# Performance work log

Measured on AMD Instinct MI355X. Metric: run time of the kernel, lower is better.

Reference implementation:

```python
import jax, jax.numpy as jnp
import numpy as np

B, S, DIM, H = 4, 2048, 1024, 16
DEPTH = DIM // H


def setup_inputs() -> dict:
    key = jax.random.key(0)
    ks = jax.random.split(key, 12)
    s = 0.02
    return {
        "Q": jax.random.normal(ks[0], (B, S, DIM), jnp.float32),
        "K": jax.random.normal(ks[1], (B, S, DIM), jnp.float32),
        "V": jax.random.normal(ks[2], (B, S, DIM), jnp.float32),
        "mask": jax.random.randint(ks[3], (B, 1, 1, S), 0, 2).astype(jnp.float32),
        "Wq": jax.random.normal(ks[4], (DIM, DIM), jnp.float32) * s,
        "bq": jnp.zeros((DIM,), jnp.float32),
        "Wk": jax.random.normal(ks[5], (DIM, DIM), jnp.float32) * s,
        "bk": jnp.zeros((DIM,), jnp.float32),
        "Wv": jax.random.normal(ks[6], (DIM, DIM), jnp.float32) * s,
        "bv": jnp.zeros((DIM,), jnp.float32),
        "Wo": jax.random.normal(ks[7], (DIM, DIM), jnp.float32) * s,
        "bo": jnp.zeros((DIM,), jnp.float32),
    }


def _split_heads(x):
    # [B,S,DIM] -> [B,H,S,DEPTH]
    return x.reshape(x.shape[0], x.shape[1], H, DEPTH).transpose(0, 2, 1, 3)


def reference(Q, K, V, mask, Wq, bq, Wk, bk, Wv, bv, Wo, bo):
    q = _split_heads(Q @ Wq + bq)
    k = _split_heads(K @ Wk + bk)
    v = _split_heads(V @ Wv + bv)
    # scaled dot-product attention; note original scales by sqrt(depth) = last dim of K after split
    logits = jnp.einsum("bhqd,bhkd->bhqk", q, k) / jnp.sqrt(jnp.float32(DEPTH))
    logits = logits + mask * -1e9
    attn = jax.nn.softmax(logits, axis=-1)
    ctx = jnp.einsum("bhqk,bhkd->bhqd", attn, v)
    ctx = ctx.transpose(0, 2, 1, 3).reshape(Q.shape[0], Q.shape[1], DIM)
    return ctx @ Wo + bo
```

## Files before the change

kernel.cpp:

```cpp
#include <hip/hip_runtime.h>

typedef short s16x8 __attribute__((ext_vector_type(8)));
typedef short s16x4 __attribute__((ext_vector_type(4)));
typedef float f32x4 __attribute__((ext_vector_type(4)));

#define MFMA32(a, b, c) __builtin_amdgcn_mfma_f32_16x16x32_bf16((a), (b), (c), 0, 0, 0)

__device__ __forceinline__ void stage16(const unsigned short* g, unsigned short* l) {
#if defined(__HIP_DEVICE_COMPILE__)
  __builtin_amdgcn_global_load_lds((const __attribute__((address_space(1))) unsigned int*)g,
                                   (__attribute__((address_space(3))) unsigned int*)l, 16, 0, 0);
#endif
}

__device__ __forceinline__ unsigned short f2b(float f) {
  unsigned int u = __builtin_bit_cast(unsigned int, f);
  unsigned int r = u + 0x7FFFu + ((u >> 16) & 1u);
  return (unsigned short)(r >> 16);
}
__device__ __forceinline__ unsigned int pk2(float a, float b) {
  return (unsigned int)f2b(a) | ((unsigned int)f2b(b) << 16);
}
__device__ __forceinline__ float fast_exp2(float x) {
#if defined(__HIP_DEVICE_COMPILE__) && __has_builtin(__builtin_amdgcn_exp2f)
  return __builtin_amdgcn_exp2f(x);
#else
  return exp2f(x);
#endif
}

__global__ __launch_bounds__(256) void castq(const float* __restrict__ X,
                                             unsigned short* __restrict__ Y) {
  int i = blockIdx.x * 256 + threadIdx.x;
  float4 f0 = ((const float4*)X)[i * 2];
  float4 f1 = ((const float4*)X)[i * 2 + 1];
  uint4 u;
  u.x = pk2(f0.x, f0.y);
  u.y = pk2(f0.z, f0.w);
  u.z = pk2(f1.x, f1.y);
  u.w = pk2(f1.z, f1.w);
  ((uint4*)Y)[i] = u;
}

__global__ void wtrans(const float* __restrict__ W0, const float* __restrict__ W1,
                       const float* __restrict__ W2, const float* __restrict__ W3,
                       unsigned short* __restrict__ T0, unsigned short* __restrict__ T1,
                       unsigned short* __restrict__ T2, unsigned short* __restrict__ T3) {
  const float* W;
  unsigned short* T;
  switch (blockIdx.z) {
    case 0: W = W0; T = T0; break;
    case 1: W = W1; T = T1; break;
    case 2: W = W2; T = T2; break;
    default: W = W3; T = T3; break;
  }
  __shared__ float tile[32][33];
  const int n0 = blockIdx.x << 5;
  const int k0 = blockIdx.y << 5;
  const int tx = threadIdx.x;
  const int ty = threadIdx.y;
#pragma unroll
  for (int j = 0; j < 4; ++j)
    tile[ty + 8 * j][tx] = W[(size_t)(k0 + ty + 8 * j) * 1024 + n0 + tx];
  __syncthreads();
#pragma unroll
  for (int j = 0; j < 4; ++j)
    T[(size_t)(n0 + ty + 8 * j) * 1024 + k0 + tx] = f2b(tile[tx][ty + 8 * j]);
}

template <int MODE>
__global__ __launch_bounds__(256, 2) void gemm_bt(const unsigned short* __restrict__ A,
                                                  const unsigned short* __restrict__ Bt,
                                                  const float* __restrict__ bias,
                                                  void* __restrict__ Cout, float oscale) {
  __shared__ __align__(16) unsigned short As[128 * 32];
  __shared__ __align__(16) unsigned short Bs[128 * 32];
  const int n0 = blockIdx.x * 128;
  const int m0 = blockIdx.y * 128;
  const int tid = threadIdx.x;
  const int w = tid >> 6;
  const int lane = tid & 63;
  const int lr = lane & 15;
  const int lg = lane >> 4;
  const int wm = (w >> 1) << 6;
  const int wn = (w & 1) << 6;

  const int srow = w * 16 + (lane >> 2);
  const int sseg = lane & 3;
  const unsigned short* Ag0 = A + (size_t)(m0 + srow) * 1024 + sseg * 8;
  const unsigned short* Ag1 = A + (size_t)(m0 + 64 + srow) * 1024 + sseg * 8;
  const unsigned short* Bg0 = Bt + (size_t)(n0 + srow) * 1024 + sseg * 8;
  const unsigned short* Bg1 = Bt + (size_t)(n0 + 64 + srow) * 1024 + sseg * 8;
  unsigned short* Al0 = &As[(w * 16) * 32];
  unsigned short* Al1 = &As[(64 + w * 16) * 32];
  unsigned short* Bl0 = &Bs[(w * 16) * 32];
  unsigned short* Bl1 = &Bs[(64 + w * 16) * 32];

  f32x4 acc[4][4];
#pragma unroll
  for (int i = 0; i < 4; ++i)
#pragma unroll
    for (int j = 0; j < 4; ++j) {
      f32x4 z = {0.f, 0.f, 0.f, 0.f};
      acc[i][j] = z;
    }

  for (int k0 = 0; k0 < 1024; k0 += 32) {
    stage16(Ag0 + k0, Al0);
    stage16(Ag1 + k0, Al1);
    stage16(Bg0 + k0, Bl0);
    stage16(Bg1 + k0, Bl1);
    __syncthreads();
    s16x8 af[4], bfr[4];
#pragma unroll
    for (int mt = 0; mt < 4; ++mt) af[mt] = *(const s16x8*)&As[(wm + mt * 16 + lr) * 32 + lg * 8];
#pragma unroll
    for (int nt = 0; nt < 4; ++nt) bfr[nt] = *(const s16x8*)&Bs[(wn + nt * 16 + lr) * 32 + lg * 8];
#pragma unroll
    for (int mt = 0; mt < 4; ++mt)
#pragma unroll
      for (int nt = 0; nt < 4; ++nt)
        acc[mt][nt] = MFMA32(af[mt], bfr[nt], acc[mt][nt]);
    __syncthreads();
  }

  float bcol[4];
#pragma unroll
  for (int nt = 0; nt < 4; ++nt) bcol[nt] = bias[n0 + wn + nt * 16 + lr];

#pragma unroll
  for (int mt = 0; mt < 4; ++mt)
#pragma unroll
    for (int nt = 0; nt < 4; ++nt)
#pragma unroll
      for (int r = 0; r < 4; ++r) {
        float v = (acc[mt][nt][r] + bcol[nt]) * oscale;
        int row = m0 + wm + mt * 16 + lg * 4 + r;
        int col = n0 + wn + nt * 16 + lr;
        if constexpr (MODE == 0) {
          int b = row >> 11, s = row & 2047, hh = col >> 6, d = col & 63;
          ((unsigned short*)Cout)[(((size_t)(b * 16 + hh) * 2048 + s) << 6) + d] = f2b(v);
        } else if constexpr (MODE == 1) {
          int b = row >> 11, s = row & 2047, hh = col >> 6, d = col & 63;
          ((unsigned short*)Cout)[(((size_t)(b * 16 + hh) * 64 + d) << 11) + s] = f2b(v);
        } else {
          ((float*)Cout)[(size_t)row * 1024 + col] = v;
        }
      }
}

__global__ __launch_bounds__(256, 4) void flash_attn(const unsigned short* __restrict__ qh,
                                                     const unsigned short* __restrict__ kh,
                                                     const unsigned short* __restrict__ vt,
                                                     const float* __restrict__ mask,
                                                     unsigned short* __restrict__ ctx) {
  const float c2 = 1.4426950408889634e9f;
  const int id = blockIdx.x;
  const int bh = id & 63;
  const int qtile = id >> 6;
  const int b = bh >> 4;
  const int h = bh & 15;
  const int q0 = qtile << 7;
  const int tid = threadIdx.x;
  const int w = tid >> 6;
  const int lane = tid & 63;
  const int lr = lane & 15;
  const int lg = lane >> 4;

  __shared__ __align__(16) unsigned short Ks[64 * 64];
  __shared__ __align__(16) unsigned short Vs[64 * 64];

  const unsigned short* qbase = qh + ((size_t)bh * 2048 + q0 + w * 32) * 64;
  const unsigned short* kbase = kh + (size_t)bh * 2048 * 64;
  const unsigned short* vbase = vt + (size_t)bh * 64 * 2048;
  const float* mbase = mask + b * 2048;

  const int rowc = lane >> 3;
  const int gseg = (lane & 7) ^ rowc;
  const unsigned short* kg0 = kbase + (size_t)(w * 16 + rowc) * 64 + gseg * 8;
  const unsigned short* kg1 = kbase + (size_t)(w * 16 + 8 + rowc) * 64 + gseg * 8;
  const unsigned short* vg0 = vbase + (size_t)(w * 16 + rowc) * 2048 + gseg * 8;
  const unsigned short* vg1 = vbase + (size_t)(w * 16 + 8 + rowc) * 2048 + gseg * 8;
  unsigned short* kl0 = &Ks[(w * 16 + 0) * 64];
  unsigned short* kl1 = &Ks[(w * 16 + 8) * 64];
  unsigned short* vl0 = &Vs[(w * 16 + 0) * 64];
  unsigned short* vl1 = &Vs[(w * 16 + 8) * 64];

  s16x8 qf[2][2];
#pragma unroll
  for (int qt = 0; qt < 2; ++qt)
#pragma unroll
    for (int kk = 0; kk < 2; ++kk)
      qf[qt][kk] = *(const s16x8*)(qbase + (qt * 16 + lr) * 64 + kk * 32 + lg * 8);

  const s16x8 ones8 = {(short)0x3F80, (short)0x3F80, (short)0x3F80, (short)0x3F80,
                       (short)0x3F80, (short)0x3F80, (short)0x3F80, (short)0x3F80};

  f32x4 o_acc[2][4];
  f32x4 l_acc[2];
#pragma unroll
  for (int qt = 0; qt < 2; ++qt) {
    f32x4 z = {0.f, 0.f, 0.f, 0.f};
    l_acc[qt] = z;
#pragma unroll
    for (int dt = 0; dt < 4; ++dt) o_acc[qt][dt] = z;
  }

  for (int t0 = 0; t0 < 2048; t0 += 64) {
    stage16(kg0 + (size_t)t0 * 64, kl0);
    stage16(kg1 + (size_t)t0 * 64, kl1);
    stage16(vg0 + t0, vl0);
    stage16(vg1 + t0, vl1);
    float4 mk[4];
#pragma unroll
    for (int kt = 0; kt < 4; ++kt) mk[kt] = *(const float4*)(mbase + t0 + kt * 16 + lg * 4);
    __syncthreads();

    const int sw = lr & 7;
    unsigned int pw[4][2][2];
#pragma unroll
    for (int kt = 0; kt < 4; ++kt) {
      const int krow = kt * 16 + lr;
      s16x8 kf0 = *(const s16x8*)&Ks[krow * 64 + ((lg ^ sw) * 8)];
      s16x8 kf1 = *(const s16x8*)&Ks[krow * 64 + (((4 + lg) ^ sw) * 8)];
      float ml0 = mk[kt].x * c2, ml1 = mk[kt].y * c2;
      float ml2 = mk[kt].z * c2, ml3 = mk[kt].w * c2;
#pragma unroll
      for (int qt = 0; qt < 2; ++qt) {
        f32x4 s = {0.f, 0.f, 0.f, 0.f};
        s = MFMA32(kf0, qf[qt][0], s);
        s = MFMA32(kf1, qf[qt][1], s);
        pw[kt][qt][0] = pk2(fast_exp2(s[0] - ml0), fast_exp2(s[1] - ml1));
        pw[kt][qt][1] = pk2(fast_exp2(s[2] - ml2), fast_exp2(s[3] - ml3));
      }
    }

#pragma unroll
    for (int c = 0; c < 2; ++c) {
      s16x8 pb[2];
#pragma unroll
      for (int qt = 0; qt < 2; ++qt) {
        uint4 u;
        u.x = pw[2 * c][qt][0];
        u.y = pw[2 * c][qt][1];
        u.z = pw[2 * c + 1][qt][0];
        u.w = pw[2 * c + 1][qt][1];
        pb[qt] = __builtin_bit_cast(s16x8, u);
        l_acc[qt] = MFMA32(ones8, pb[qt], l_acc[qt]);
      }
      const int plo = ((c << 2) | (lg >> 1)) ^ sw;
      const int phi = ((c << 2) | 2 | (lg >> 1)) ^ sw;
      const int sub = (lg & 1) * 4;
#pragma unroll
      for (int dt = 0; dt < 4; ++dt) {
        const int d = dt * 16 + lr;
        s16x4 vlo = *(const s16x4*)&Vs[d * 64 + plo * 8 + sub];
        s16x4 vhi = *(const s16x4*)&Vs[d * 64 + phi * 8 + sub];
        s16x8 vf = __builtin_shufflevector(vlo, vhi, 0, 1, 2, 3, 4, 5, 6, 7);
#pragma unroll
        for (int qt = 0; qt < 2; ++qt) o_acc[qt][dt] = MFMA32(vf, pb[qt], o_acc[qt][dt]);
      }
    }
    __syncthreads();
  }

#pragma unroll
  for (int qt = 0; qt < 2; ++qt) {
    float inv = 1.0f / l_acc[qt][0];
    int q = q0 + w * 32 + qt * 16 + lr;
    unsigned short* cp = ctx + ((size_t)(b * 2048 + q) * 16 + h) * 64 + lg * 4;
#pragma unroll
    for (int dt = 0; dt < 4; ++dt) {
      f32x4 o = o_acc[qt][dt];
      uint2 u;
      u.x = pk2(o[0] * inv, o[1] * inv);
      u.y = pk2(o[2] * inv, o[3] * inv);
      *(uint2*)(cp + dt * 16) = u;
    }
  }
}

extern "C" void kernel_launch(void* const* d_in, const int* in_sizes, int n_in,
                              void* d_out, int out_size, void* d_ws, size_t ws_size,
                              hipStream_t stream) {
  (void)in_sizes; (void)n_in; (void)out_size; (void)ws_size;
  const float* Q = (const float*)d_in[0];
  const float* K = (const float*)d_in[1];
  const float* V = (const float*)d_in[2];
  const float* mask = (const float*)d_in[3];
  const float* Wq = (const float*)d_in[4];
  const float* bq = (const float*)d_in[5];
  const float* Wk = (const float*)d_in[6];
  const float* bk = (const float*)d_in[7];
  const float* Wv = (const float*)d_in[8];
  const float* bv = (const float*)d_in[9];
  const float* Wo = (const float*)d_in[10];
  const float* bo = (const float*)d_in[11];

  char* ws = (char*)d_ws;
  unsigned short* wqt = (unsigned short*)(ws + (size_t)0);
  unsigned short* wkt = (unsigned short*)(ws + ((size_t)2 << 20));
  unsigned short* wvt = (unsigned short*)(ws + ((size_t)4 << 20));
  unsigned short* wot = (unsigned short*)(ws + ((size_t)6 << 20));
  unsigned short* qhb = (unsigned short*)(ws + ((size_t)8 << 20));
  unsigned short* khb = (unsigned short*)(ws + ((size_t)24 << 20));
  unsigned short* vtb = (unsigned short*)(ws + ((size_t)40 << 20));
  unsigned short* tmp = (unsigned short*)(ws + ((size_t)56 << 20));
  unsigned short* ctx = tmp;

  wtrans<<<dim3(32, 32, 4), dim3(32, 8), 0, stream>>>(Wq, Wk, Wv, Wo, wqt, wkt, wvt, wot);

  const float qscale = 0.18033688011112042f;
  dim3 gg(8, 64), bb(256);
  const int castBlocks = (8192 * 1024) / (256 * 8);

  castq<<<castBlocks, 256, 0, stream>>>(Q, tmp);
  gemm_bt<0><<<gg, bb, 0, stream>>>(tmp, wqt, bq, qhb, qscale);
  castq<<<castBlocks, 256, 0, stream>>>(K, tmp);
  gemm_bt<0><<<gg, bb, 0, stream>>>(tmp, wkt, bk, khb, 1.0f);
  castq<<<castBlocks, 256, 0, stream>>>(V, tmp);
  gemm_bt<1><<<gg, bb, 0, stream>>>(tmp, wvt, bv, vtb, 1.0f);

  flash_attn<<<dim3(1024), dim3(256), 0, stream>>>(qhb, khb, vtb, mask, ctx);

  gemm_bt<2><<<gg, bb, 0, stream>>>(ctx, wot, bo, d_out, 1.0f);
}
```

Baseline: 389.0 us.

## Double-buffer K/V tiles in flash attention and use perm-based bf16 packing

Adds a second LDS buffer for K and V, so the next tile is prefetched with async global-to-LDS loads while the current tile is computed, and each iteration ends with a single vmcnt wait plus barrier instead of two syncthreads. It also rewrites the bf16 pair packing to use a byte-permute instruction rather than separate shifts and ORs. LDS use per block doubles to 32KB, which may limit occupancy under the four-blocks-per-CU launch bound. The mask loads are also covered by the vmcnt(0) wait.

```diff
diff --git a/kernel.cpp b/kernel.cpp
--- a/kernel.cpp
+++ b/kernel.cpp
@@ -19,7 +19,15 @@
   return (unsigned short)(r >> 16);
 }
 __device__ __forceinline__ unsigned int pk2(float a, float b) {
+#if defined(__HIP_DEVICE_COMPILE__)
+  unsigned int ua = __builtin_bit_cast(unsigned int, a);
+  unsigned int ub = __builtin_bit_cast(unsigned int, b);
+  ua += 0x7FFFu + ((ua >> 16) & 1u);
+  ub += 0x7FFFu + ((ub >> 16) & 1u);
+  return __builtin_amdgcn_perm(ub, ua, 0x07060302u);
+#else
   return (unsigned int)f2b(a) | ((unsigned int)f2b(b) << 16);
+#endif
 }
 __device__ __forceinline__ float fast_exp2(float x) {
 #if defined(__HIP_DEVICE_COMPILE__) && __has_builtin(__builtin_amdgcn_exp2f)
@@ -167,8 +175,8 @@
   const int lr = lane & 15;
   const int lg = lane >> 4;
 
-  __shared__ __align__(16) unsigned short Ks[64 * 64];
-  __shared__ __align__(16) unsigned short Vs[64 * 64];
+  __shared__ __align__(16) unsigned short Ks[2 * 64 * 64];
+  __shared__ __align__(16) unsigned short Vs[2 * 64 * 64];
 
   const unsigned short* qbase = qh + ((size_t)bh * 2048 + q0 + w * 32) * 64;
   const unsigned short* kbase = kh + (size_t)bh * 2048 * 64;
@@ -206,23 +214,33 @@
     for (int dt = 0; dt < 4; ++dt) o_acc[qt][dt] = z;
   }
 
+  stage16(kg0, kl0);
+  stage16(kg1, kl1);
+  stage16(vg0, vl0);
+  stage16(vg1, vl1);
+  asm volatile("s_waitcnt vmcnt(0)\n\ts_barrier" ::: "memory");
+
+  int cur = 0;
   for (int t0 = 0; t0 < 2048; t0 += 64) {
-    stage16(kg0 + (size_t)t0 * 64, kl0);
-    stage16(kg1 + (size_t)t0 * 64, kl1);
-    stage16(vg0 + t0, vl0);
-    stage16(vg1 + t0, vl1);
+    if (t0 + 64 < 2048) {
+      const int nb = (cur ^ 1) * 4096;
+      stage16(kg0 + (size_t)(t0 + 64) * 64, kl0 + nb);
+      stage16(kg1 + (size_t)(t0 + 64) * 64, kl1 + nb);
+      stage16(vg0 + (t0 + 64), vl0 + nb);
+      stage16(vg1 + (t0 + 64), vl1 + nb);
+    }
     float4 mk[4];
 #pragma unroll
     for (int kt = 0; kt < 4; ++kt) mk[kt] = *(const float4*)(mbase + t0 + kt * 16 + lg * 4);
-    __syncthreads();
-
+
+    const int cb = cur * 4096;
     const int sw = lr & 7;
     unsigned int pw[4][2][2];
 #pragma unroll
     for (int kt = 0; kt < 4; ++kt) {
       const int krow = kt * 16 + lr;
-      s16x8 kf0 = *(const s16x8*)&Ks[krow * 64 + ((lg ^ sw) * 8)];
-      s16x8 kf1 = *(const s16x8*)&Ks[krow * 64 + (((4 + lg) ^ sw) * 8)];
+      s16x8 kf0 = *(const s16x8*)&Ks[cb + krow * 64 + ((lg ^ sw) * 8)];
+      s16x8 kf1 = *(const s16x8*)&Ks[cb + krow * 64 + (((4 + lg) ^ sw) * 8)];
       float ml0 = mk[kt].x * c2, ml1 = mk[kt].y * c2;
       float ml2 = mk[kt].z * c2, ml3 = mk[kt].w * c2;
 #pragma unroll
@@ -254,14 +272,16 @@
 #pragma unroll
       for (int dt = 0; dt < 4; ++dt) {
         const int d = dt * 16 + lr;
-        s16x4 vlo = *(const s16x4*)&Vs[d * 64 + plo * 8 + sub];
-        s16x4 vhi = *(const s16x4*)&Vs[d * 64 + phi * 8 + sub];
+        s16x4 vlo = *(const s16x4*)&Vs[cb + d * 64 + plo * 8 + sub];
+        s16x4 vhi = *(const s16x4*)&Vs[cb + d * 64 + phi * 8 + sub];
         s16x8 vf = __builtin_shufflevector(vlo, vhi, 0, 1, 2, 3, 4, 5, 6, 7);
 #pragma unroll
         for (int qt = 0; qt < 2; ++qt) o_acc[qt][dt] = MFMA32(vf, pb[qt], o_acc[qt][dt]);
       }
     }
-    __syncthreads();
+
+    asm volatile("s_waitcnt vmcnt(0)\n\ts_barrier" ::: "memory");
+    cur ^= 1;
   }
 
 #pragma unroll
```

Result: faster. 381.3 us (-2.0%).
